# Performance work log

Measured on AMD Instinct MI355X. Metric: run time of the kernel, lower is better.

## Reference

```python
import jax, jax.numpy as jnp
import numpy as np

D = 256      # input channels
DK = 64      # key/query/value channels
BS, W, H = 8, 64, 64


def setup_inputs() -> dict:
    key = jax.random.key(0)
    k1, k2, k3, k4 = jax.random.split(key, 4)
    v = jax.random.normal(k1, (BS, D, W, H), dtype=jnp.float32)
    # conv1x1 weights collapse to plain matrices over the channel dim
    Wqkv = jax.random.normal(k2, (3 * DK, D), dtype=jnp.float32) * 0.02
    Wout = jax.random.normal(k3, (D, DK), dtype=jnp.float32) * 0.02
    gamma = jax.random.normal(k4, (1,), dtype=jnp.float32)  # original inits to 0; nonzero for a non-degenerate baseline
    return {"v": v, "Wqkv": Wqkv, "Wout": Wout, "gamma": gamma}


def reference(v, Wqkv, Wout, gamma):
    bs, c, w, h = v.shape
    n = w * h
    d_k = Wout.shape[1]
    x = v.reshape(bs, c, n)                      # (b, c, n)
    qkv = jnp.einsum('oc,bcn->bon', Wqkv, x)      # 1x1 conv == channel matmul
    q = qkv[:, :d_k]                              # (b, dk, n)
    k = qkv[:, d_k:2 * d_k]
    val = qkv[:, 2 * d_k:]
    s = jnp.einsum('bdi,bdj->bij', q, k)          # (b, n, n) = query^T key
    beta = jax.nn.softmax(s, axis=2)              # exp(s - logsumexp(s, axis=2))
    y = jnp.einsum('bdi,bij->bdj', val, beta)     # bmm(value, beta)
    o = jnp.einsum('od,bdn->bon', Wout, y) * gamma[0] + x
    return o.reshape(bs, c, w, h)
```

## Files before the change

kernel.cpp:

```cpp
#include <hip/hip_runtime.h>

typedef unsigned short ushort_t;
typedef __bf16 bf16x8 __attribute__((ext_vector_type(8)));
typedef short short4v __attribute__((ext_vector_type(4)));
typedef float f32x4 __attribute__((ext_vector_type(4)));
typedef unsigned int uint4v __attribute__((ext_vector_type(4)));
typedef unsigned int uint2v __attribute__((ext_vector_type(2)));

#define NTOK 4096
#define DMODEL 256
#define DK 64
#define BS 8
#define LN2INV 1.44269504088896f

__device__ __forceinline__ ushort_t f2bf(float f) {
  unsigned u = __builtin_bit_cast(unsigned, f);
  u += 0x7fffu + ((u >> 16) & 1u);
  return (ushort_t)(u >> 16);
}
__device__ __forceinline__ float bf2f(ushort_t s) {
  return __builtin_bit_cast(float, ((unsigned)s) << 16);
}
__device__ __forceinline__ bf16x8 lds_frag(const ushort_t* p) {
  return __builtin_bit_cast(bf16x8, *(const uint4v*)p);
}
__device__ __forceinline__ float fexp2(float x) {
#if __has_builtin(__builtin_amdgcn_exp2f)
  return __builtin_amdgcn_exp2f(x);
#else
  return exp2f(x);
#endif
}
__device__ __forceinline__ unsigned bfpack(float x, float y) {
  return __builtin_amdgcn_perm(__builtin_bit_cast(unsigned, y),
                               __builtin_bit_cast(unsigned, x), 0x07060302u);
}
__device__ __forceinline__ f32x4 mfma16(short4v a, short4v b, f32x4 c) {
#if defined(__HIP_DEVICE_COMPILE__)
#if __has_builtin(__builtin_amdgcn_mfma_f32_16x16x16bf16_1k)
  return __builtin_amdgcn_mfma_f32_16x16x16bf16_1k(a, b, c, 0, 0, 0);
#else
  typedef __bf16 bf16x4 __attribute__((ext_vector_type(4)));
  return __builtin_amdgcn_mfma_f32_16x16x16_bf16(__builtin_bit_cast(bf16x4, a),
                                                 __builtin_bit_cast(bf16x4, b), c, 0, 0, 0);
#endif
#else
  (void)a; (void)b;
  return c;
#endif
}

__global__ __launch_bounds__(256) void k_convert(const float* __restrict__ Wqkv,
                                                 const float* __restrict__ Wout,
                                                 ushort_t* __restrict__ Wb,
                                                 ushort_t* __restrict__ Woutb) {
  int i = blockIdx.x * 256 + threadIdx.x;
  if (i < 3 * DK * DMODEL) {
    float w = Wqkv[i];
    if (i < DK * DMODEL) w *= LN2INV;
    Wb[i] = f2bf(w);
  } else {
    int j = i - 3 * DK * DMODEL;
    Woutb[j] = f2bf(Wout[j]);
  }
}

__global__ __launch_bounds__(256) void k_transpose(const float* __restrict__ x,
                                                   ushort_t* __restrict__ xT) {
  const int b = blockIdx.z;
  const int c0 = blockIdx.y * 64;
  const int n0 = blockIdx.x * 64;
  const int tid = threadIdx.x;
  __shared__ __align__(16) ushort_t t[64 * 72];
  const float* xb = x + (size_t)b * DMODEL * NTOK;
  ushort_t* xTb = xT + (size_t)b * NTOK * DMODEL;
#pragma unroll
  for (int kr = 0; kr < 2; kr++) {
    int s = tid + 256 * kr;
    int c = s >> 3, ns = (s & 7) * 8;
    const float* src = xb + (size_t)(c0 + c) * NTOK + n0 + ns;
    f32x4 a = *(const f32x4*)src;
    f32x4 bq = *(const f32x4*)(src + 4);
    uint4v o;
    o.x = (unsigned)f2bf(a[0]) | ((unsigned)f2bf(a[1]) << 16);
    o.y = (unsigned)f2bf(a[2]) | ((unsigned)f2bf(a[3]) << 16);
    o.z = (unsigned)f2bf(bq[0]) | ((unsigned)f2bf(bq[1]) << 16);
    o.w = (unsigned)f2bf(bq[2]) | ((unsigned)f2bf(bq[3]) << 16);
    *(uint4v*)(t + c * 72 + ns) = o;
  }
  __syncthreads();
#pragma unroll
  for (int kr = 0; kr < 2; kr++) {
    int s = tid + 256 * kr;
    int n = s >> 3, cs = (s & 7) * 8;
    unsigned e0 = t[(cs + 0) * 72 + n], e1 = t[(cs + 1) * 72 + n];
    unsigned e2 = t[(cs + 2) * 72 + n], e3 = t[(cs + 3) * 72 + n];
    unsigned e4 = t[(cs + 4) * 72 + n], e5 = t[(cs + 5) * 72 + n];
    unsigned e6 = t[(cs + 6) * 72 + n], e7 = t[(cs + 7) * 72 + n];
    uint4v o;
    o.x = e0 | (e1 << 16); o.y = e2 | (e3 << 16);
    o.z = e4 | (e5 << 16); o.w = e6 | (e7 << 16);
    *(uint4v*)(xTb + (size_t)(n0 + n) * DMODEL + c0 + cs) = o;
  }
}

__global__ __launch_bounds__(256) void k_qkv(const ushort_t* __restrict__ xT,
                                             const ushort_t* __restrict__ W,
                                             ushort_t* __restrict__ QT,
                                             ushort_t* __restrict__ KT,
                                             ushort_t* __restrict__ Vv) {
  const int b = blockIdx.y;
  const int n0 = blockIdx.x * 64;
  const int tid = threadIdx.x;
  const int lane = tid & 63, wv = tid >> 6;
  const int quad = lane >> 4, l15 = lane & 15;
  __shared__ __align__(16) ushort_t lw[192 * 40];
  __shared__ __align__(16) ushort_t lx[64 * 40];
  f32x4 acc[3][4];
  const f32x4 zero4 = {0.f, 0.f, 0.f, 0.f};
#pragma unroll
  for (int i = 0; i < 3; i++)
#pragma unroll
    for (int j = 0; j < 4; j++) acc[i][j] = zero4;

  const ushort_t* xTb = xT + ((size_t)b * NTOK + n0) * DMODEL;

  for (int c0 = 0; c0 < DMODEL; c0 += 32) {
    __syncthreads();
#pragma unroll
    for (int kr = 0; kr < 3; kr++) {
      int s = tid + 256 * kr;
      int o = s >> 2, cs = (s & 3) * 8;
      *(uint4v*)(lw + o * 40 + cs) = *(const uint4v*)(W + o * DMODEL + c0 + cs);
    }
    {
      int n = tid >> 2, cs = (tid & 3) * 8;
      *(uint4v*)(lx + n * 40 + cs) = *(const uint4v*)(xTb + (size_t)n * DMODEL + c0 + cs);
    }
    __syncthreads();
    bf16x8 bb[4];
#pragma unroll
    for (int nt = 0; nt < 4; nt++) bb[nt] = lds_frag(lx + (nt * 16 + l15) * 40 + quad * 8);
#pragma unroll
    for (int mt = 0; mt < 3; mt++) {
      bf16x8 a = lds_frag(lw + (wv * 48 + mt * 16 + l15) * 40 + quad * 8);
#pragma unroll
      for (int nt = 0; nt < 4; nt++)
        acc[mt][nt] = __builtin_amdgcn_mfma_f32_16x16x32_bf16(a, bb[nt], acc[mt][nt], 0, 0, 0);
    }
  }
#pragma unroll
  for (int mt = 0; mt < 3; mt++) {
    int o = wv * 48 + mt * 16 + quad * 4;
#pragma unroll
    for (int nt = 0; nt < 4; nt++) {
      int n = n0 + nt * 16 + l15;
      f32x4 v4 = acc[mt][nt];
      if (o < 128) {
        ushort_t* dst = (o < 64) ? (QT + ((size_t)b * NTOK + n) * DK + o)
                                 : (KT + ((size_t)b * NTOK + n) * DK + (o - 64));
        uint2v ww;
        ww.x = (unsigned)f2bf(v4[0]) | ((unsigned)f2bf(v4[1]) << 16);
        ww.y = (unsigned)f2bf(v4[2]) | ((unsigned)f2bf(v4[3]) << 16);
        *(uint2v*)dst = ww;
      } else {
        int d = o - 128;
#pragma unroll
        for (int r = 0; r < 4; r++)
          Vv[((size_t)b * DK + d + r) * NTOK + n] = f2bf(v4[r]);
      }
    }
  }
}

__global__ __launch_bounds__(256) void k_rsum(const ushort_t* __restrict__ QT,
                                              const ushort_t* __restrict__ KT,
                                              float* __restrict__ Rp) {
  const int id = blockIdx.x;
  const int b = id & 7;
  const int rest = id >> 3;
  const int i0 = (rest & 63) * 64;
  const int jh = rest >> 6;
  const int tid = threadIdx.x;
  const int lane = tid & 63, wv = tid >> 6;
  const int quad = lane >> 4, l15 = lane & 15;
  __shared__ __align__(16) ushort_t lk[2][64 * 72];
  const ushort_t* QTb = QT + ((size_t)b * NTOK + i0) * DK;
  const ushort_t* KTb = KT + ((size_t)b * NTOK + jh * 2048) * DK;

  const int qoff = (wv * 16 + l15) * DK + quad * 8;
  bf16x8 a0 = __builtin_bit_cast(bf16x8, *(const uint4v*)(QTb + qoff));
  bf16x8 a1 = __builtin_bit_cast(bf16x8, *(const uint4v*)(QTb + qoff + 32));

  const int sr0 = tid >> 3, sr1 = sr0 + 32;
  const int c8 = (tid & 7) * 8;

  *(uint4v*)(lk[0] + sr0 * 72 + c8) = *(const uint4v*)(KTb + (size_t)sr0 * DK + c8);
  *(uint4v*)(lk[0] + sr1 * 72 + c8) = *(const uint4v*)(KTb + (size_t)sr1 * DK + c8);
  __syncthreads();

  float ls0 = 0.f, ls1 = 0.f, ls2 = 0.f, ls3 = 0.f;
  const f32x4 zero4 = {0.f, 0.f, 0.f, 0.f};

  for (int it = 0; it < 32; it++) {
    uint4v p0, p1;
    if (it + 1 < 32) {
      const ushort_t* src = KTb + (size_t)(it + 1) * 64 * DK;
      p0 = *(const uint4v*)(src + (size_t)sr0 * DK + c8);
      p1 = *(const uint4v*)(src + (size_t)sr1 * DK + c8);
    }
    const ushort_t* kb = lk[it & 1];
#pragma unroll
    for (int nt = 0; nt < 4; nt++) {
      bf16x8 b0 = lds_frag(kb + (nt * 16 + l15) * 72 + quad * 8);
      bf16x8 b1 = lds_frag(kb + (nt * 16 + l15) * 72 + 32 + quad * 8);
      f32x4 s4 = __builtin_amdgcn_mfma_f32_16x16x32_bf16(a0, b0, zero4, 0, 0, 0);
      s4 = __builtin_amdgcn_mfma_f32_16x16x32_bf16(a1, b1, s4, 0, 0, 0);
      ls0 += fexp2(s4[0]);
      ls1 += fexp2(s4[1]);
      ls2 += fexp2(s4[2]);
      ls3 += fexp2(s4[3]);
    }
    if (it + 1 < 32) {
      ushort_t* dstb = lk[(it + 1) & 1];
      *(uint4v*)(dstb + sr0 * 72 + c8) = p0;
      *(uint4v*)(dstb + sr1 * 72 + c8) = p1;
    }
    __syncthreads();
  }

#pragma unroll
  for (int off = 1; off < 16; off <<= 1) {
    ls0 += __shfl_xor(ls0, off);
    ls1 += __shfl_xor(ls1, off);
    ls2 += __shfl_xor(ls2, off);
    ls3 += __shfl_xor(ls3, off);
  }
  if (l15 < 4) {
    float v = (l15 == 0) ? ls0 : (l15 == 1) ? ls1 : (l15 == 2) ? ls2 : ls3;
    Rp[((size_t)(jh * 8 + b)) * NTOK + i0 + wv * 16 + quad * 4 + l15] = v;
  }
}

__global__ __launch_bounds__(256) void k_rmerge(const float* __restrict__ Rp,
                                                float* __restrict__ Rr) {
  int g = blockIdx.x * 256 + threadIdx.x;
  float s = Rp[g] + Rp[BS * NTOK + g];
  Rr[g] = -__log2f(s);
}

__global__ __launch_bounds__(256) void k_pv(const ushort_t* __restrict__ QT,
                                            const ushort_t* __restrict__ KT,
                                            const ushort_t* __restrict__ Vv,
                                            const float* __restrict__ Rr,
                                            ushort_t* __restrict__ Yp) {
  const int id = blockIdx.x;
  const int b = id & 7;
  const int rest = id >> 3;
  const int j0 = (rest & 63) * 64;
  const int ih = rest >> 6;
  const int tid = threadIdx.x;
  const int lane = tid & 63, wv = tid >> 6;
  const int quad = lane >> 4, l15 = lane & 15;

  __shared__ __align__(16) ushort_t pool[18432];
#define LQ(buf) (pool + (buf) * 4608)
#define LV(buf) (pool + 9216 + (buf) * 4608)
  float* rbuf = (float*)pool;
  ushort_t* pbuf = pool + 8704;

  const ushort_t* KTb = KT + ((size_t)b * NTOK + j0) * DK;
  const ushort_t* QTb = QT + ((size_t)b * NTOK + ih * 2048) * DK;
  const ushort_t* Vbb = Vv + (size_t)b * DK * NTOK + ih * 2048;
  const float* Rrb = Rr + (size_t)b * NTOK + ih * 2048;

  bf16x8 kb0[4], kb1[4];
#pragma unroll
  for (int nt = 0; nt < 4; nt++) {
    const ushort_t* kp = KTb + (size_t)(nt * 16 + l15) * DK + quad * 8;
    kb0[nt] = __builtin_bit_cast(bf16x8, *(const uint4v*)kp);
    kb1[nt] = __builtin_bit_cast(bf16x8, *(const uint4v*)(kp + 32));
  }

  const int sr0 = tid >> 3, sr1 = sr0 + 32;
  const int c8 = (tid & 7) * 8;

  *(uint4v*)(LQ(0) + sr0 * 72 + c8) = *(const uint4v*)(QTb + (size_t)sr0 * DK + c8);
  *(uint4v*)(LQ(0) + sr1 * 72 + c8) = *(const uint4v*)(QTb + (size_t)sr1 * DK + c8);
  *(uint4v*)(LV(0) + sr0 * 72 + c8) = *(const uint4v*)(Vbb + (size_t)sr0 * NTOK + c8);
  *(uint4v*)(LV(0) + sr1 * 72 + c8) = *(const uint4v*)(Vbb + (size_t)sr1 * NTOK + c8);
  __syncthreads();

  f32x4 yt[4][4];
  const f32x4 zero4 = {0.f, 0.f, 0.f, 0.f};
#pragma unroll
  for (int i = 0; i < 4; i++)
#pragma unroll
    for (int j = 0; j < 4; j++) yt[i][j] = zero4;

  for (int it = 0; it < 32; it++) {
    const int cb = it & 1, nb = cb ^ 1;
    f32x4 lrv = *(const f32x4*)(Rrb + it * 64 + wv * 16 + quad * 4);
    uint4v q0, q1, v0, v1;
    if (it + 1 < 32) {
      const ushort_t* qsrc = QTb + (size_t)(it + 1) * 64 * DK;
      q0 = *(const uint4v*)(qsrc + (size_t)sr0 * DK + c8);
      q1 = *(const uint4v*)(qsrc + (size_t)sr1 * DK + c8);
      v0 = *(const uint4v*)(Vbb + (size_t)sr0 * NTOK + (it + 1) * 64 + c8);
      v1 = *(const uint4v*)(Vbb + (size_t)sr1 * NTOK + (it + 1) * 64 + c8);
    }
    bf16x8 a0 = lds_frag(LQ(cb) + (wv * 16 + l15) * 72 + quad * 8);
    bf16x8 a1 = lds_frag(LQ(cb) + (wv * 16 + l15) * 72 + 32 + quad * 8);
    short4v vf[4];
#pragma unroll
    for (int dsub = 0; dsub < 4; dsub++)
      vf[dsub] = __builtin_bit_cast(short4v,
          *(const uint2v*)(LV(cb) + (dsub * 16 + l15) * 72 + wv * 16 + quad * 4));
#pragma unroll
    for (int nt = 0; nt < 4; nt++) {
      f32x4 s4 = __builtin_amdgcn_mfma_f32_16x16x32_bf16(a0, kb0[nt], lrv, 0, 0, 0);
      s4 = __builtin_amdgcn_mfma_f32_16x16x32_bf16(a1, kb1[nt], s4, 0, 0, 0);
      uint2v wp;
      wp.x = bfpack(fexp2(s4[0]), fexp2(s4[1]));
      wp.y = bfpack(fexp2(s4[2]), fexp2(s4[3]));
      short4v wf = __builtin_bit_cast(short4v, wp);
#pragma unroll
      for (int dsub = 0; dsub < 4; dsub++)
        yt[nt][dsub] = mfma16(wf, vf[dsub], yt[nt][dsub]);
    }
    if (it + 1 < 32) {
      *(uint4v*)(LQ(nb) + sr0 * 72 + c8) = q0;
      *(uint4v*)(LQ(nb) + sr1 * 72 + c8) = q1;
      *(uint4v*)(LV(nb) + sr0 * 72 + c8) = v0;
      *(uint4v*)(LV(nb) + sr1 * 72 + c8) = v1;
    }
    __syncthreads();
  }

  if (wv == 0) {
#pragma unroll
    for (int nt = 0; nt < 4; nt++)
#pragma unroll
      for (int dsub = 0; dsub < 4; dsub++)
        *(f32x4*)(rbuf + (dsub * 16 + l15) * 68 + nt * 16 + quad * 4) = yt[nt][dsub];
  }
  __syncthreads();
  if (wv == 1) {
#pragma unroll
    for (int nt = 0; nt < 4; nt++)
#pragma unroll
      for (int dsub = 0; dsub < 4; dsub++) {
        float* p = rbuf + (dsub * 16 + l15) * 68 + nt * 16 + quad * 4;
        *(f32x4*)p = *(const f32x4*)p + yt[nt][dsub];
      }
  }
  __syncthreads();
  if (wv == 2) {
#pragma unroll
    for (int nt = 0; nt < 4; nt++)
#pragma unroll
      for (int dsub = 0; dsub < 4; dsub++) {
        float* p = rbuf + (dsub * 16 + l15) * 68 + nt * 16 + quad * 4;
        *(f32x4*)p = *(const f32x4*)p + yt[nt][dsub];
      }
  }
  __syncthreads();
  if (wv == 3) {
#pragma unroll
    for (int nt = 0; nt < 4; nt++)
#pragma unroll
      for (int dsub = 0; dsub < 4; dsub++) {
        const float* p = rbuf + (dsub * 16 + l15) * 68 + nt * 16 + quad * 4;
        f32x4 v4 = *(const f32x4*)p + yt[nt][dsub];
#pragma unroll
        for (int r = 0; r < 4; r++)
          pbuf[(nt * 16 + quad * 4 + r) * 72 + dsub * 16 + l15] = f2bf(v4[r]);
      }
  }
  __syncthreads();

  ushort_t* Ypb = Yp + ((size_t)(ih * 8 + b) * NTOK + j0) * DK;
#pragma unroll
  for (int kr = 0; kr < 2; kr++) {
    int s = tid + 256 * kr;
    int row = s >> 3, cc = (s & 7) * 8;
    *(uint4v*)(Ypb + (size_t)row * DK + cc) = *(const uint4v*)(pbuf + row * 72 + cc);
  }
#undef LQ
#undef LV
}

__global__ __launch_bounds__(256) void k_out(const ushort_t* __restrict__ Yp,
                                             const ushort_t* __restrict__ Wout,
                                             const float* __restrict__ gammap,
                                             const float* __restrict__ x,
                                             float* __restrict__ outp) {
  const int id = blockIdx.x;
  const int b = id & 7;
  const int n0 = (id >> 3) * 64;
  const int tid = threadIdx.x;
  const int lane = tid & 63, wv = tid >> 6;
  const int quad = lane >> 4, l15 = lane & 15;
  __shared__ __align__(16) ushort_t pbuf[64 * 72];

  const ushort_t* Y0 = Yp + ((size_t)b * NTOK + n0) * DK;
  const ushort_t* Y1 = Yp + ((size_t)(8 + b) * NTOK + n0) * DK;
#pragma unroll
  for (int kr = 0; kr < 2; kr++) {
    int s = tid + 256 * kr;
    int row = s >> 3, c8 = (s & 7) * 8;
    uint4v ua = *(const uint4v*)(Y0 + (size_t)row * DK + c8);
    uint4v ub = *(const uint4v*)(Y1 + (size_t)row * DK + c8);
    uint4v oc;
    unsigned* pa = (unsigned*)&ua;
    unsigned* pb = (unsigned*)&ub;
    unsigned* po = (unsigned*)&oc;
#pragma unroll
    for (int w = 0; w < 4; w++) {
      float lo = bf2f((ushort_t)(pa[w] & 0xffff)) + bf2f((ushort_t)(pb[w] & 0xffff));
      float hi = bf2f((ushort_t)(pa[w] >> 16)) + bf2f((ushort_t)(pb[w] >> 16));
      po[w] = bfpack(lo, hi);
    }
    *(uint4v*)(pbuf + row * 72 + c8) = oc;
  }
  __syncthreads();

  const f32x4 zero4 = {0.f, 0.f, 0.f, 0.f};
  bf16x8 yb0[4], yb1[4];
#pragma unroll
  for (int nt = 0; nt < 4; nt++) {
    yb0[nt] = lds_frag(pbuf + (nt * 16 + l15) * 72 + quad * 8);
    yb1[nt] = lds_frag(pbuf + (nt * 16 + l15) * 72 + 32 + quad * 8);
  }
  f32x4 oacc[4][4];
#pragma unroll
  for (int m = 0; m < 4; m++)
#pragma unroll
    for (int nt = 0; nt < 4; nt++) oacc[m][nt] = zero4;
#pragma unroll
  for (int m = 0; m < 4; m++) {
    int c = (wv * 4 + m) * 16 + l15;
    bf16x8 aw0 = __builtin_bit_cast(bf16x8, *(const uint4v*)(Wout + c * DK + quad * 8));
    bf16x8 aw1 = __builtin_bit_cast(bf16x8, *(const uint4v*)(Wout + c * DK + 32 + quad * 8));
#pragma unroll
    for (int nt = 0; nt < 4; nt++) {
      oacc[m][nt] = __builtin_amdgcn_mfma_f32_16x16x32_bf16(aw0, yb0[nt], oacc[m][nt], 0, 0, 0);
      oacc[m][nt] = __builtin_amdgcn_mfma_f32_16x16x32_bf16(aw1, yb1[nt], oacc[m][nt], 0, 0, 0);
    }
  }
  float g = gammap[0];
  const float* xb = x + (size_t)b * DMODEL * NTOK;
  float* ob = outp + (size_t)b * DMODEL * NTOK;
#pragma unroll
  for (int m = 0; m < 4; m++) {
    int cbase = (wv * 4 + m) * 16 + quad * 4;
#pragma unroll
    for (int nt = 0; nt < 4; nt++) {
      int n = n0 + nt * 16 + l15;
#pragma unroll
      for (int r = 0; r < 4; r++) {
        size_t idx = (size_t)(cbase + r) * NTOK + n;
        ob[idx] = oacc[m][nt][r] * g + xb[idx];
      }
    }
  }
}

extern "C" void kernel_launch(void* const* d_in, const int* in_sizes, int n_in,
                              void* d_out, int out_size, void* d_ws, size_t ws_size,
                              hipStream_t stream) {
  const float* v = (const float*)d_in[0];
  const float* Wqkv = (const float*)d_in[1];
  const float* Wout = (const float*)d_in[2];
  const float* gamma = (const float*)d_in[3];
  float* outp = (float*)d_out;

  ushort_t* xT = (ushort_t*)d_ws;
  ushort_t* QT = xT + (size_t)BS * NTOK * DMODEL;
  ushort_t* KT = QT + (size_t)BS * NTOK * DK;
  ushort_t* Vs = KT + (size_t)BS * NTOK * DK;
  ushort_t* Wb = Vs + (size_t)BS * DK * NTOK;
  ushort_t* Woutb = Wb + 3 * DK * DMODEL;
  float* Rp = (float*)(Woutb + DMODEL * DK);
  float* Rr = Rp + 2 * (size_t)BS * NTOK;
  ushort_t* Yp = (ushort_t*)(Rr + (size_t)BS * NTOK);

  k_convert<<<dim3(256), 256, 0, stream>>>(Wqkv, Wout, Wb, Woutb);
  k_transpose<<<dim3(64, 4, BS), 256, 0, stream>>>(v, xT);
  k_qkv<<<dim3(64, BS), 256, 0, stream>>>(xT, Wb, QT, KT, Vs);
  k_rsum<<<dim3(1024), 256, 0, stream>>>(QT, KT, Rp);
  k_rmerge<<<dim3(128), 256, 0, stream>>>(Rp, Rr);
  k_pv<<<dim3(1024), 256, 0, stream>>>(QT, KT, Vs, Rr, Yp);
  k_out<<<dim3(512), 256, 0, stream>>>(Yp, Woutb, gamma, v, outp);
}
```

Before: 220.5 us.

## Deepen global prefetch to two tiles and use raw barriers in attention kernels

Both the row-sum and PV attention loops are restructured as manually unrolled ping-pong phases. Global loads are now issued two tiles ahead, and the LDS store for the next tile is placed before the compute instead of after it. The __syncthreads calls are replaced by an lgkmcnt wait plus s_barrier, so outstanding global loads need not drain at each barrier. k_pv also gets launch_bounds(256,3) and s_setprio around its MFMA section, and it prefetches the Rr vector one iteration ahead. The cost is higher register pressure, and the occupancy hint may force spills.

Result: slower. 229.5 us (+4.1%).

```diff
diff --git a/kernel.cpp b/kernel.cpp
--- a/kernel.cpp
+++ b/kernel.cpp
@@ -194,40 +194,55 @@
 
   const int sr0 = tid >> 3, sr1 = sr0 + 32;
   const int c8 = (tid & 7) * 8;
-
-  *(uint4v*)(lk[0] + sr0 * 72 + c8) = *(const uint4v*)(KTb + (size_t)sr0 * DK + c8);
-  *(uint4v*)(lk[0] + sr1 * 72 + c8) = *(const uint4v*)(KTb + (size_t)sr1 * DK + c8);
-  __syncthreads();
+  ushort_t* LK0 = lk[0];
+  ushort_t* LK1 = lk[1];
+
+  {
+    uint4v t0 = *(const uint4v*)(KTb + (size_t)sr0 * DK + c8);
+    uint4v t1 = *(const uint4v*)(KTb + (size_t)sr1 * DK + c8);
+    *(uint4v*)(LK0 + sr0 * 72 + c8) = t0;
+    *(uint4v*)(LK0 + sr1 * 72 + c8) = t1;
+  }
+  uint4v pA0 = *(const uint4v*)(KTb + (size_t)(64 + sr0) * DK + c8);
+  uint4v pA1 = *(const uint4v*)(KTb + (size_t)(64 + sr1) * DK + c8);
+  uint4v pB0, pB1;
+  asm volatile("s_waitcnt lgkmcnt(0)" ::: "memory");
+  __builtin_amdgcn_s_barrier();
+  asm volatile("" ::: "memory");
 
   float ls0 = 0.f, ls1 = 0.f, ls2 = 0.f, ls3 = 0.f;
   const f32x4 zero4 = {0.f, 0.f, 0.f, 0.f};
 
-  for (int it = 0; it < 32; it++) {
-    uint4v p0, p1;
-    if (it + 1 < 32) {
-      const ushort_t* src = KTb + (size_t)(it + 1) * 64 * DK;
-      p0 = *(const uint4v*)(src + (size_t)sr0 * DK + c8);
-      p1 = *(const uint4v*)(src + (size_t)sr1 * DK + c8);
-    }
-    const ushort_t* kb = lk[it & 1];
-#pragma unroll
-    for (int nt = 0; nt < 4; nt++) {
-      bf16x8 b0 = lds_frag(kb + (nt * 16 + l15) * 72 + quad * 8);
-      bf16x8 b1 = lds_frag(kb + (nt * 16 + l15) * 72 + 32 + quad * 8);
-      f32x4 s4 = __builtin_amdgcn_mfma_f32_16x16x32_bf16(a0, b0, zero4, 0, 0, 0);
-      s4 = __builtin_amdgcn_mfma_f32_16x16x32_bf16(a1, b1, s4, 0, 0, 0);
-      ls0 += fexp2(s4[0]);
-      ls1 += fexp2(s4[1]);
-      ls2 += fexp2(s4[2]);
-      ls3 += fexp2(s4[3]);
-    }
-    if (it + 1 < 32) {
-      ushort_t* dstb = lk[(it + 1) & 1];
-      *(uint4v*)(dstb + sr0 * 72 + c8) = p0;
-      *(uint4v*)(dstb + sr1 * 72 + c8) = p1;
-    }
-    __syncthreads();
-  }
+#define RS_PHASE(LKc, LKn, pW0, pW1, pN0, pN1, itv)                                      \
+  {                                                                                      \
+    const int tpre = ((itv) + 2 < 32) ? (itv) + 2 : 31;                                  \
+    pN0 = *(const uint4v*)(KTb + (size_t)(tpre * 64 + sr0) * DK + c8);                   \
+    pN1 = *(const uint4v*)(KTb + (size_t)(tpre * 64 + sr1) * DK + c8);                   \
+    asm volatile("" ::: "memory");                                                       \
+    if ((itv) + 1 < 32) {                                                                \
+      *(uint4v*)(LKn + sr0 * 72 + c8) = pW0;                                             \
+      *(uint4v*)(LKn + sr1 * 72 + c8) = pW1;                                             \
+    }                                                                                    \
+    _Pragma("unroll") for (int nt = 0; nt < 4; nt++) {                                   \
+      bf16x8 b0 = lds_frag(LKc + (nt * 16 + l15) * 72 + quad * 8);                       \
+      bf16x8 b1 = lds_frag(LKc + (nt * 16 + l15) * 72 + 32 + quad * 8);                  \
+      f32x4 s4 = __builtin_amdgcn_mfma_f32_16x16x32_bf16(a0, b0, zero4, 0, 0, 0);        \
+      s4 = __builtin_amdgcn_mfma_f32_16x16x32_bf16(a1, b1, s4, 0, 0, 0);                 \
+      ls0 += fexp2(s4[0]);                                                               \
+      ls1 += fexp2(s4[1]);                                                               \
+      ls2 += fexp2(s4[2]);                                                               \
+      ls3 += fexp2(s4[3]);                                                               \
+    }                                                                                    \
+    asm volatile("s_waitcnt lgkmcnt(0)" ::: "memory");                                   \
+    __builtin_amdgcn_s_barrier();                                                       \
+    asm volatile("" ::: "memory");                                                       \
+  }
+
+  for (int itb = 0; itb < 32; itb += 2) {
+    RS_PHASE(LK0, LK1, pA0, pA1, pB0, pB1, itb);
+    RS_PHASE(LK1, LK0, pB0, pB1, pA0, pA1, itb + 1);
+  }
+#undef RS_PHASE
 
 #pragma unroll
   for (int off = 1; off < 16; off <<= 1) {
@@ -249,11 +264,11 @@
   Rr[g] = -__log2f(s);
 }
 
-__global__ __launch_bounds__(256) void k_pv(const ushort_t* __restrict__ QT,
-                                            const ushort_t* __restrict__ KT,
-                                            const ushort_t* __restrict__ Vv,
-                                            const float* __restrict__ Rr,
-                                            ushort_t* __restrict__ Yp) {
+__global__ __launch_bounds__(256, 3) void k_pv(const ushort_t* __restrict__ QT,
+                                               const ushort_t* __restrict__ KT,
+                                               const ushort_t* __restrict__ Vv,
+                                               const float* __restrict__ Rr,
+                                               ushort_t* __restrict__ Yp) {
   const int id = blockIdx.x;
   const int b = id & 7;
   const int rest = id >> 3;
@@ -264,8 +279,10 @@
   const int quad = lane >> 4, l15 = lane & 15;
 
   __shared__ __align__(16) ushort_t pool[18432];
-#define LQ(buf) (pool + (buf) * 4608)
-#define LV(buf) (pool + 9216 + (buf) * 4608)
+  ushort_t* LQ0 = pool;
+  ushort_t* LQ1 = pool + 4608;
+  ushort_t* LV0 = pool + 9216;
+  ushort_t* LV1 = pool + 13824;
   float* rbuf = (float*)pool;
   ushort_t* pbuf = pool + 8704;
 
@@ -284,12 +301,27 @@
 
   const int sr0 = tid >> 3, sr1 = sr0 + 32;
   const int c8 = (tid & 7) * 8;
-
-  *(uint4v*)(LQ(0) + sr0 * 72 + c8) = *(const uint4v*)(QTb + (size_t)sr0 * DK + c8);
-  *(uint4v*)(LQ(0) + sr1 * 72 + c8) = *(const uint4v*)(QTb + (size_t)sr1 * DK + c8);
-  *(uint4v*)(LV(0) + sr0 * 72 + c8) = *(const uint4v*)(Vbb + (size_t)sr0 * NTOK + c8);
-  *(uint4v*)(LV(0) + sr1 * 72 + c8) = *(const uint4v*)(Vbb + (size_t)sr1 * NTOK + c8);
-  __syncthreads();
+  const int voff = wv * 16 + quad * 4;
+
+  {
+    uint4v t0 = *(const uint4v*)(QTb + (size_t)sr0 * DK + c8);
+    uint4v t1 = *(const uint4v*)(QTb + (size_t)sr1 * DK + c8);
+    uint4v t2 = *(const uint4v*)(Vbb + (size_t)sr0 * NTOK + c8);
+    uint4v t3 = *(const uint4v*)(Vbb + (size_t)sr1 * NTOK + c8);
+    *(uint4v*)(LQ0 + sr0 * 72 + c8) = t0;
+    *(uint4v*)(LQ0 + sr1 * 72 + c8) = t1;
+    *(uint4v*)(LV0 + sr0 * 72 + c8) = t2;
+    *(uint4v*)(LV0 + sr1 * 72 + c8) = t3;
+  }
+  uint4v qA0 = *(const uint4v*)(QTb + (size_t)(64 + sr0) * DK + c8);
+  uint4v qA1 = *(const uint4v*)(QTb + (size_t)(64 + sr1) * DK + c8);
+  uint4v vA0 = *(const uint4v*)(Vbb + (size_t)sr0 * NTOK + 64 + c8);
+  uint4v vA1 = *(const uint4v*)(Vbb + (size_t)sr1 * NTOK + 64 + c8);
+  uint4v qB0, qB1, vB0, vB1;
+  f32x4 lrcur = *(const f32x4*)(Rrb + voff);
+  asm volatile("s_waitcnt lgkmcnt(0)" ::: "memory");
+  __builtin_amdgcn_s_barrier();
+  asm volatile("" ::: "memory");
 
   f32x4 yt[4][4];
   const f32x4 zero4 = {0.f, 0.f, 0.f, 0.f};
@@ -298,45 +330,53 @@
 #pragma unroll
     for (int j = 0; j < 4; j++) yt[i][j] = zero4;
 
-  for (int it = 0; it < 32; it++) {
-    const int cb = it & 1, nb = cb ^ 1;
-    f32x4 lrv = *(const f32x4*)(Rrb + it * 64 + wv * 16 + quad * 4);
-    uint4v q0, q1, v0, v1;
-    if (it + 1 < 32) {
-      const ushort_t* qsrc = QTb + (size_t)(it + 1) * 64 * DK;
-      q0 = *(const uint4v*)(qsrc + (size_t)sr0 * DK + c8);
-      q1 = *(const uint4v*)(qsrc + (size_t)sr1 * DK + c8);
-      v0 = *(const uint4v*)(Vbb + (size_t)sr0 * NTOK + (it + 1) * 64 + c8);
-      v1 = *(const uint4v*)(Vbb + (size_t)sr1 * NTOK + (it + 1) * 64 + c8);
-    }
-    bf16x8 a0 = lds_frag(LQ(cb) + (wv * 16 + l15) * 72 + quad * 8);
-    bf16x8 a1 = lds_frag(LQ(cb) + (wv * 16 + l15) * 72 + 32 + quad * 8);
-    short4v vf[4];
-#pragma unroll
-    for (int dsub = 0; dsub < 4; dsub++)
-      vf[dsub] = __builtin_bit_cast(short4v,
-          *(const uint2v*)(LV(cb) + (dsub * 16 + l15) * 72 + wv * 16 + quad * 4));
-#pragma unroll
-    for (int nt = 0; nt < 4; nt++) {
-      f32x4 s4 = __builtin_amdgcn_mfma_f32_16x16x32_bf16(a0, kb0[nt], lrv, 0, 0, 0);
-      s4 = __builtin_amdgcn_mfma_f32_16x16x32_bf16(a1, kb1[nt], s4, 0, 0, 0);
-      uint2v wp;
-      wp.x = bfpack(fexp2(s4[0]), fexp2(s4[1]));
-      wp.y = bfpack(fexp2(s4[2]), fexp2(s4[3]));
-      short4v wf = __builtin_bit_cast(short4v, wp);
-#pragma unroll
-      for (int dsub = 0; dsub < 4; dsub++)
-        yt[nt][dsub] = mfma16(wf, vf[dsub], yt[nt][dsub]);
-    }
-    if (it + 1 < 32) {
-      *(uint4v*)(LQ(nb) + sr0 * 72 + c8) = q0;
-      *(uint4v*)(LQ(nb) + sr1 * 72 + c8) = q1;
-      *(uint4v*)(LV(nb) + sr0 * 72 + c8) = v0;
-      *(uint4v*)(LV(nb) + sr1 * 72 + c8) = v1;
-    }
-    __syncthreads();
-  }
-
+#define PV_PHASE(LQc, LVc, LQn, LVn, qW0, qW1, vW0, vW1, qN0, qN1, vN0, vN1, itv)        \
+  {                                                                                      \
+    const int tpre = ((itv) + 2 < 32) ? (itv) + 2 : 31;                                  \
+    const int tlr = ((itv) + 1 < 32) ? (itv) + 1 : 31;                                   \
+    qN0 = *(const uint4v*)(QTb + (size_t)(tpre * 64 + sr0) * DK + c8);                   \
+    qN1 = *(const uint4v*)(QTb + (size_t)(tpre * 64 + sr1) * DK + c8);                   \
+    vN0 = *(const uint4v*)(Vbb + (size_t)sr0 * NTOK + tpre * 64 + c8);                   \
+    vN1 = *(const uint4v*)(Vbb + (size_t)sr1 * NTOK + tpre * 64 + c8);                   \
+    f32x4 lrnew = *(const f32x4*)(Rrb + tlr * 64 + voff);                                \
+    asm volatile("" ::: "memory");                                                       \
+    bf16x8 a0 = lds_frag(LQc + (wv * 16 + l15) * 72 + quad * 8);                         \
+    bf16x8 a1 = lds_frag(LQc + (wv * 16 + l15) * 72 + 32 + quad * 8);                    \
+    short4v vf[4];                                                                       \
+    _Pragma("unroll") for (int dsub = 0; dsub < 4; dsub++)                               \
+        vf[dsub] = __builtin_bit_cast(short4v,                                           \
+            *(const uint2v*)(LVc + (dsub * 16 + l15) * 72 + wv * 16 + quad * 4));        \
+    if ((itv) + 1 < 32) {                                                                \
+      *(uint4v*)(LQn + sr0 * 72 + c8) = qW0;                                             \
+      *(uint4v*)(LQn + sr1 * 72 + c8) = qW1;                                             \
+      *(uint4v*)(LVn + sr0 * 72 + c8) = vW0;                                             \
+      *(uint4v*)(LVn + sr1 * 72 + c8) = vW1;                                             \
+    }                                                                                    \
+    __builtin_amdgcn_s_setprio(1);                                                       \
+    _Pragma("unroll") for (int nt = 0; nt < 4; nt++) {                                   \
+      f32x4 s4 = __builtin_amdgcn_mfma_f32_16x16x32_bf16(a0, kb0[nt], lrcur, 0, 0, 0);   \
+      s4 = __builtin_amdgcn_mfma_f32_16x16x32_bf16(a1, kb1[nt], s4, 0, 0, 0);            \
+      uint2v wp;                                                                         \
+      wp.x = bfpack(fexp2(s4[0]), fexp2(s4[1]));                                         \
+      wp.y = bfpack(fexp2(s4[2]), fexp2(s4[3]));                                         \
+      short4v wf = __builtin_bit_cast(short4v, wp);                                      \
+      _Pragma("unroll") for (int dsub = 0; dsub < 4; dsub++)                             \
+          yt[nt][dsub] = mfma16(wf, vf[dsub], yt[nt][dsub]);                             \
+    }                                                                                    \
+    __builtin_amdgcn_s_setprio(0);                                                       \
+    asm volatile("s_waitcnt lgkmcnt(0)" ::: "memory");                                   \
+    __builtin_amdgcn_s_barrier();                                                       \
+    asm volatile("" ::: "memory");                                                       \
+    lrcur = lrnew;                                                                       \
+  }
+
+  for (int itb = 0; itb < 32; itb += 2) {
+    PV_PHASE(LQ0, LV0, LQ1, LV1, qA0, qA1, vA0, vA1, qB0, qB1, vB0, vB1, itb);
+    PV_PHASE(LQ1, LV1, LQ0, LV0, qB0, qB1, vB0, vB1, qA0, qA1, vA0, vA1, itb + 1);
+  }
+#undef PV_PHASE
+
+  __syncthreads();
   if (wv == 0) {
 #pragma unroll
     for (int nt = 0; nt < 4; nt++)
@@ -386,8 +426,6 @@
     int row = s >> 3, cc = (s & 7) * 8;
     *(uint4v*)(Ypb + (size_t)row * DK + cc) = *(const uint4v*)(pbuf + row * 72 + cc);
   }
-#undef LQ
-#undef LV
 }
 
 __global__ __launch_bounds__(256) void k_out(const ushort_t* __restrict__ Yp,
```

## Drop LDS staging in attention kernels; load fragments directly from global memory

Applied to the files above, without the earlier changes.

k_rsum now has each wave handle a separate quarter of the key range for all 64 queries, loading K fragments straight from global memory. This removes the LDS double buffer and the per-iteration barriers, and produces eight partial row sums that k_rmerge adds together. k_qkv writes V in a fragment-ordered tiled layout so k_pv can load MFMA operands with two 16-byte global loads per iteration instead of staging Q and V through LDS. The costs are more redundant global/L2 traffic and exposed load latency without software prefetch. The partial-sum buffer reuses the xT workspace, which is safe only because xT is dead after k_qkv.

After: 212.1 us. 3.8% less time.

```diff
diff --git a/kernel.cpp b/kernel.cpp
--- a/kernel.cpp
+++ b/kernel.cpp
@@ -23,6 +23,17 @@
 }
 __device__ __forceinline__ bf16x8 lds_frag(const ushort_t* p) {
   return __builtin_bit_cast(bf16x8, *(const uint4v*)p);
+}
+__device__ __forceinline__ bf16x8 ldg8(const ushort_t* p) {
+  return __builtin_bit_cast(bf16x8, *(const uint4v*)p);
+}
+__device__ __forceinline__ short4v lo8(uint4v v) {
+  uint2v t; t.x = v.x; t.y = v.y;
+  return __builtin_bit_cast(short4v, t);
+}
+__device__ __forceinline__ short4v hi8(uint4v v) {
+  uint2v t; t.x = v.z; t.y = v.w;
+  return __builtin_bit_cast(short4v, t);
 }
 __device__ __forceinline__ float fexp2(float x) {
 #if __has_builtin(__builtin_amdgcn_exp2f)
@@ -108,7 +119,7 @@
                                              const ushort_t* __restrict__ W,
                                              ushort_t* __restrict__ QT,
                                              ushort_t* __restrict__ KT,
-                                             ushort_t* __restrict__ Vv) {
+                                             ushort_t* __restrict__ Vf) {
   const int b = blockIdx.y;
   const int n0 = blockIdx.x * 64;
   const int tid = threadIdx.x;
@@ -164,18 +175,20 @@
         ww.y = (unsigned)f2bf(v4[2]) | ((unsigned)f2bf(v4[3]) << 16);
         *(uint2v*)dst = ww;
       } else {
-        int d = o - 128;
-#pragma unroll
-        for (int r = 0; r < 4; r++)
-          Vv[((size_t)b * DK + d + r) * NTOK + n] = f2bf(v4[r]);
-      }
-    }
-  }
-}
-
-__global__ __launch_bounds__(256) void k_rsum(const ushort_t* __restrict__ QT,
-                                              const ushort_t* __restrict__ KT,
-                                              float* __restrict__ Rp) {
+        int dbase = o - 128;
+        size_t tbase = ((((size_t)b * 64 + (n0 >> 6)) * 4 + nt) * 2 + (dbase >> 5)) * 512;
+        ushort_t* vp = Vf + tbase + ((l15 >> 2) << 7) + ((dbase & 15) << 3) +
+                       (((dbase >> 4) & 1) << 2) + (l15 & 3);
+#pragma unroll
+        for (int r = 0; r < 4; r++) vp[r << 3] = f2bf(v4[r]);
+      }
+    }
+  }
+}
+
+__global__ __launch_bounds__(256, 4) void k_rsum(const ushort_t* __restrict__ QT,
+                                                 const ushort_t* __restrict__ KT,
+                                                 float* __restrict__ Rp) {
   const int id = blockIdx.x;
   const int b = id & 7;
   const int rest = id >> 3;
@@ -184,76 +197,78 @@
   const int tid = threadIdx.x;
   const int lane = tid & 63, wv = tid >> 6;
   const int quad = lane >> 4, l15 = lane & 15;
-  __shared__ __align__(16) ushort_t lk[2][64 * 72];
   const ushort_t* QTb = QT + ((size_t)b * NTOK + i0) * DK;
-  const ushort_t* KTb = KT + ((size_t)b * NTOK + jh * 2048) * DK;
-
-  const int qoff = (wv * 16 + l15) * DK + quad * 8;
-  bf16x8 a0 = __builtin_bit_cast(bf16x8, *(const uint4v*)(QTb + qoff));
-  bf16x8 a1 = __builtin_bit_cast(bf16x8, *(const uint4v*)(QTb + qoff + 32));
-
-  const int sr0 = tid >> 3, sr1 = sr0 + 32;
-  const int c8 = (tid & 7) * 8;
-
-  *(uint4v*)(lk[0] + sr0 * 72 + c8) = *(const uint4v*)(KTb + (size_t)sr0 * DK + c8);
-  *(uint4v*)(lk[0] + sr1 * 72 + c8) = *(const uint4v*)(KTb + (size_t)sr1 * DK + c8);
-  __syncthreads();
-
-  float ls0 = 0.f, ls1 = 0.f, ls2 = 0.f, ls3 = 0.f;
+  const ushort_t* KTb = KT + ((size_t)b * NTOK + jh * 2048 + wv * 512) * DK;
+
+  bf16x8 aq0[4], aq1[4];
+#pragma unroll
+  for (int isub = 0; isub < 4; isub++) {
+    const ushort_t* qp = QTb + (size_t)(isub * 16 + l15) * DK + quad * 8;
+    aq0[isub] = ldg8(qp);
+    aq1[isub] = ldg8(qp + 32);
+  }
+
+  f32x4 racc[4];
   const f32x4 zero4 = {0.f, 0.f, 0.f, 0.f};
-
-  for (int it = 0; it < 32; it++) {
-    uint4v p0, p1;
-    if (it + 1 < 32) {
-      const ushort_t* src = KTb + (size_t)(it + 1) * 64 * DK;
-      p0 = *(const uint4v*)(src + (size_t)sr0 * DK + c8);
-      p1 = *(const uint4v*)(src + (size_t)sr1 * DK + c8);
-    }
-    const ushort_t* kb = lk[it & 1];
+#pragma unroll
+  for (int isub = 0; isub < 4; isub++) racc[isub] = zero4;
+
+#pragma unroll 1
+  for (int ph = 0; ph < 8; ph++) {
+    const ushort_t* kb_base = KTb + (size_t)ph * 64 * DK;
+    bf16x8 kb0[4], kb1[4];
 #pragma unroll
     for (int nt = 0; nt < 4; nt++) {
-      bf16x8 b0 = lds_frag(kb + (nt * 16 + l15) * 72 + quad * 8);
-      bf16x8 b1 = lds_frag(kb + (nt * 16 + l15) * 72 + 32 + quad * 8);
-      f32x4 s4 = __builtin_amdgcn_mfma_f32_16x16x32_bf16(a0, b0, zero4, 0, 0, 0);
-      s4 = __builtin_amdgcn_mfma_f32_16x16x32_bf16(a1, b1, s4, 0, 0, 0);
-      ls0 += fexp2(s4[0]);
-      ls1 += fexp2(s4[1]);
-      ls2 += fexp2(s4[2]);
-      ls3 += fexp2(s4[3]);
-    }
-    if (it + 1 < 32) {
-      ushort_t* dstb = lk[(it + 1) & 1];
-      *(uint4v*)(dstb + sr0 * 72 + c8) = p0;
-      *(uint4v*)(dstb + sr1 * 72 + c8) = p1;
-    }
-    __syncthreads();
-  }
-
-#pragma unroll
-  for (int off = 1; off < 16; off <<= 1) {
-    ls0 += __shfl_xor(ls0, off);
-    ls1 += __shfl_xor(ls1, off);
-    ls2 += __shfl_xor(ls2, off);
-    ls3 += __shfl_xor(ls3, off);
-  }
-  if (l15 < 4) {
-    float v = (l15 == 0) ? ls0 : (l15 == 1) ? ls1 : (l15 == 2) ? ls2 : ls3;
-    Rp[((size_t)(jh * 8 + b)) * NTOK + i0 + wv * 16 + quad * 4 + l15] = v;
+      const ushort_t* kp = kb_base + (size_t)(nt * 16 + l15) * DK + quad * 8;
+      kb0[nt] = ldg8(kp);
+      kb1[nt] = ldg8(kp + 32);
+    }
+#pragma unroll
+    for (int isub = 0; isub < 4; isub++)
+#pragma unroll
+      for (int nt = 0; nt < 4; nt++) {
+        f32x4 s4 = __builtin_amdgcn_mfma_f32_16x16x32_bf16(aq0[isub], kb0[nt], zero4, 0, 0, 0);
+        s4 = __builtin_amdgcn_mfma_f32_16x16x32_bf16(aq1[isub], kb1[nt], s4, 0, 0, 0);
+        racc[isub][0] += fexp2(s4[0]);
+        racc[isub][1] += fexp2(s4[1]);
+        racc[isub][2] += fexp2(s4[2]);
+        racc[isub][3] += fexp2(s4[3]);
+      }
+  }
+
+#pragma unroll
+  for (int isub = 0; isub < 4; isub++)
+#pragma unroll
+    for (int r = 0; r < 4; r++) {
+      float v = racc[isub][r];
+      v += __shfl_xor(v, 1);
+      v += __shfl_xor(v, 2);
+      v += __shfl_xor(v, 4);
+      v += __shfl_xor(v, 8);
+      racc[isub][r] = v;
+    }
+  if (l15 == 0) {
+    float* dst = Rp + ((size_t)(jh * 4 + wv) * BS + b) * NTOK + i0;
+#pragma unroll
+    for (int isub = 0; isub < 4; isub++)
+      *(f32x4*)(dst + isub * 16 + quad * 4) = racc[isub];
   }
 }
 
 __global__ __launch_bounds__(256) void k_rmerge(const float* __restrict__ Rp,
                                                 float* __restrict__ Rr) {
   int g = blockIdx.x * 256 + threadIdx.x;
-  float s = Rp[g] + Rp[BS * NTOK + g];
+  float s = 0.f;
+#pragma unroll
+  for (int p = 0; p < 8; p++) s += Rp[(size_t)p * BS * NTOK + g];
   Rr[g] = -__log2f(s);
 }
 
-__global__ __launch_bounds__(256) void k_pv(const ushort_t* __restrict__ QT,
-                                            const ushort_t* __restrict__ KT,
-                                            const ushort_t* __restrict__ Vv,
-                                            const float* __restrict__ Rr,
-                                            ushort_t* __restrict__ Yp) {
+__global__ __launch_bounds__(256, 4) void k_pv(const ushort_t* __restrict__ QT,
+                                               const ushort_t* __restrict__ KT,
+                                               const ushort_t* __restrict__ Vf,
+                                               const float* __restrict__ Rr,
+                                               ushort_t* __restrict__ Yp) {
   const int id = blockIdx.x;
   const int b = id & 7;
   const int rest = id >> 3;
@@ -263,33 +278,22 @@
   const int lane = tid & 63, wv = tid >> 6;
   const int quad = lane >> 4, l15 = lane & 15;
 
-  __shared__ __align__(16) ushort_t pool[18432];
-#define LQ(buf) (pool + (buf) * 4608)
-#define LV(buf) (pool + 9216 + (buf) * 4608)
+  __shared__ __align__(16) ushort_t pool[13312];
   float* rbuf = (float*)pool;
   ushort_t* pbuf = pool + 8704;
 
   const ushort_t* KTb = KT + ((size_t)b * NTOK + j0) * DK;
   const ushort_t* QTb = QT + ((size_t)b * NTOK + ih * 2048) * DK;
-  const ushort_t* Vbb = Vv + (size_t)b * DK * NTOK + ih * 2048;
+  const ushort_t* Vfb = Vf + ((size_t)b * 64 + ih * 32) * 4096;
   const float* Rrb = Rr + (size_t)b * NTOK + ih * 2048;
 
   bf16x8 kb0[4], kb1[4];
 #pragma unroll
   for (int nt = 0; nt < 4; nt++) {
     const ushort_t* kp = KTb + (size_t)(nt * 16 + l15) * DK + quad * 8;
-    kb0[nt] = __builtin_bit_cast(bf16x8, *(const uint4v*)kp);
-    kb1[nt] = __builtin_bit_cast(bf16x8, *(const uint4v*)(kp + 32));
-  }
-
-  const int sr0 = tid >> 3, sr1 = sr0 + 32;
-  const int c8 = (tid & 7) * 8;
-
-  *(uint4v*)(LQ(0) + sr0 * 72 + c8) = *(const uint4v*)(QTb + (size_t)sr0 * DK + c8);
-  *(uint4v*)(LQ(0) + sr1 * 72 + c8) = *(const uint4v*)(QTb + (size_t)sr1 * DK + c8);
-  *(uint4v*)(LV(0) + sr0 * 72 + c8) = *(const uint4v*)(Vbb + (size_t)sr0 * NTOK + c8);
-  *(uint4v*)(LV(0) + sr1 * 72 + c8) = *(const uint4v*)(Vbb + (size_t)sr1 * NTOK + c8);
-  __syncthreads();
+    kb0[nt] = ldg8(kp);
+    kb1[nt] = ldg8(kp + 32);
+  }
 
   f32x4 yt[4][4];
   const f32x4 zero4 = {0.f, 0.f, 0.f, 0.f};
@@ -298,24 +302,19 @@
 #pragma unroll
     for (int j = 0; j < 4; j++) yt[i][j] = zero4;
 
+  const int qrow = (wv * 16 + l15) * DK + quad * 8;
+  const int vfo = wv * 1024 + lane * 8;
+
+#pragma unroll 1
   for (int it = 0; it < 32; it++) {
-    const int cb = it & 1, nb = cb ^ 1;
+    const ushort_t* qp = QTb + (size_t)it * 64 * DK + qrow;
+    bf16x8 a0 = ldg8(qp);
+    bf16x8 a1 = ldg8(qp + 32);
+    const ushort_t* vp = Vfb + (size_t)it * 4096 + vfo;
+    uint4v vv0 = *(const uint4v*)vp;
+    uint4v vv1 = *(const uint4v*)(vp + 512);
     f32x4 lrv = *(const f32x4*)(Rrb + it * 64 + wv * 16 + quad * 4);
-    uint4v q0, q1, v0, v1;
-    if (it + 1 < 32) {
-      const ushort_t* qsrc = QTb + (size_t)(it + 1) * 64 * DK;
-      q0 = *(const uint4v*)(qsrc + (size_t)sr0 * DK + c8);
-      q1 = *(const uint4v*)(qsrc + (size_t)sr1 * DK + c8);
-      v0 = *(const uint4v*)(Vbb + (size_t)sr0 * NTOK + (it + 1) * 64 + c8);
-      v1 = *(const uint4v*)(Vbb + (size_t)sr1 * NTOK + (it + 1) * 64 + c8);
-    }
-    bf16x8 a0 = lds_frag(LQ(cb) + (wv * 16 + l15) * 72 + quad * 8);
-    bf16x8 a1 = lds_frag(LQ(cb) + (wv * 16 + l15) * 72 + 32 + quad * 8);
-    short4v vf[4];
-#pragma unroll
-    for (int dsub = 0; dsub < 4; dsub++)
-      vf[dsub] = __builtin_bit_cast(short4v,
-          *(const uint2v*)(LV(cb) + (dsub * 16 + l15) * 72 + wv * 16 + quad * 4));
+    short4v vf0 = lo8(vv0), vf1 = hi8(vv0), vf2 = lo8(vv1), vf3 = hi8(vv1);
 #pragma unroll
     for (int nt = 0; nt < 4; nt++) {
       f32x4 s4 = __builtin_amdgcn_mfma_f32_16x16x32_bf16(a0, kb0[nt], lrv, 0, 0, 0);
@@ -324,17 +323,11 @@
       wp.x = bfpack(fexp2(s4[0]), fexp2(s4[1]));
       wp.y = bfpack(fexp2(s4[2]), fexp2(s4[3]));
       short4v wf = __builtin_bit_cast(short4v, wp);
-#pragma unroll
-      for (int dsub = 0; dsub < 4; dsub++)
-        yt[nt][dsub] = mfma16(wf, vf[dsub], yt[nt][dsub]);
-    }
-    if (it + 1 < 32) {
-      *(uint4v*)(LQ(nb) + sr0 * 72 + c8) = q0;
-      *(uint4v*)(LQ(nb) + sr1 * 72 + c8) = q1;
-      *(uint4v*)(LV(nb) + sr0 * 72 + c8) = v0;
-      *(uint4v*)(LV(nb) + sr1 * 72 + c8) = v1;
-    }
-    __syncthreads();
+      yt[nt][0] = mfma16(wf, vf0, yt[nt][0]);
+      yt[nt][1] = mfma16(wf, vf1, yt[nt][1]);
+      yt[nt][2] = mfma16(wf, vf2, yt[nt][2]);
+      yt[nt][3] = mfma16(wf, vf3, yt[nt][3]);
+    }
   }
 
   if (wv == 0) {
@@ -386,8 +379,6 @@
     int row = s >> 3, cc = (s & 7) * 8;
     *(uint4v*)(Ypb + (size_t)row * DK + cc) = *(const uint4v*)(pbuf + row * 72 + cc);
   }
-#undef LQ
-#undef LV
 }
 
 __global__ __launch_bounds__(256) void k_out(const ushort_t* __restrict__ Yp,
@@ -478,18 +469,19 @@
   ushort_t* xT = (ushort_t*)d_ws;
   ushort_t* QT = xT + (size_t)BS * NTOK * DMODEL;
   ushort_t* KT = QT + (size_t)BS * NTOK * DK;
-  ushort_t* Vs = KT + (size_t)BS * NTOK * DK;
-  ushort_t* Wb = Vs + (size_t)BS * DK * NTOK;
+  ushort_t* Vf = KT + (size_t)BS * NTOK * DK;
+  ushort_t* Wb = Vf + (size_t)BS * DK * NTOK;
   ushort_t* Woutb = Wb + 3 * DK * DMODEL;
-  float* Rp = (float*)(Woutb + DMODEL * DK);
-  float* Rr = Rp + 2 * (size_t)BS * NTOK;
+  float* RpOld = (float*)(Woutb + DMODEL * DK);
+  float* Rr = RpOld + 2 * (size_t)BS * NTOK;
   ushort_t* Yp = (ushort_t*)(Rr + (size_t)BS * NTOK);
+  float* Rp = (float*)xT;
 
   k_convert<<<dim3(256), 256, 0, stream>>>(Wqkv, Wout, Wb, Woutb);
   k_transpose<<<dim3(64, 4, BS), 256, 0, stream>>>(v, xT);
-  k_qkv<<<dim3(64, BS), 256, 0, stream>>>(xT, Wb, QT, KT, Vs);
+  k_qkv<<<dim3(64, BS), 256, 0, stream>>>(xT, Wb, QT, KT, Vf);
   k_rsum<<<dim3(1024), 256, 0, stream>>>(QT, KT, Rp);
   k_rmerge<<<dim3(128), 256, 0, stream>>>(Rp, Rr);
-  k_pv<<<dim3(1024), 256, 0, stream>>>(QT, KT, Vs, Rr, Yp);
+  k_pv<<<dim3(1024), 256, 0, stream>>>(QT, KT, Vf, Rr, Yp);
   k_out<<<dim3(512), 256, 0, stream>>>(Yp, Woutb, gamma, v, outp);
 }
```
